# Optimization experiments

Measured on AMD Instinct MI355X. Metric: run time of the kernel, lower is better.

Reference implementation:

```python
import jax, jax.numpy as jnp
import numpy as np

K, D = 8, 32          # num_heads, node_out_dim
KD = K * D            # 256
NEG = 0.2             # LeakyReLU negative slope
N, E = 100000, 300000
DIN, DREL = 128, 64


def setup_inputs() -> dict:
    key = jax.random.key(0)
    ks = iter(jax.random.split(key, 64))
    def nrm(shape, scale):
        return jax.random.normal(next(ks), shape, jnp.float32) * scale
    inp = {}
    # per-relation target-node features feats[(s,e,d)] : (N_d, d_in)
    for nm in ["feat_ui", "feat_iu", "feat_ii", "feat_ii_rev"]:
        inp[nm] = nrm((N, DIN), 1.0)
    # relation input features (d_rel,)
    for nm in ["r_ui", "r_iu", "r_ii", "r_ii_rev"]:
        inp[nm] = nrm((DREL,), 1.0)
    # fc_node per ntype (no bias), shared for src/dst roles
    inp["W_user"] = nrm((DIN, KD), 0.05)
    inp["W_item"] = nrm((DIN, KD), 0.05)
    # fc_rel per etype (no bias): d_rel -> 2*K*d
    for nm in ["Wrel_ui", "Wrel_iu", "Wrel_ii", "Wrel_ii_rev"]:
        inp[nm] = nrm((DREL, 2 * KD), 0.05)
    # cross-relation attention vectors (K, d)
    for nm in ["attn_ui", "attn_iu", "attn_ii", "attn_ii_rev"]:
        inp[nm] = nrm((K, D), 0.1)
    # residual fc per ntype (with bias) and residual gate scalar
    inp["Wres_user"] = nrm((DIN, KD), 0.05); inp["bres_user"] = nrm((KD,), 0.02)
    inp["Wres_item"] = nrm((DIN, KD), 0.05); inp["bres_item"] = nrm((KD,), 0.02)
    inp["a_user"] = jax.random.uniform(next(ks), (1,), jnp.float32)
    inp["a_item"] = jax.random.uniform(next(ks), (1,), jnp.float32)
    # fc_upd per etype (with bias): d_rel -> K*rel_out
    for nm in ["ui", "iu", "ii", "ii_rev"]:
        inp["Wupd_" + nm] = nrm((DREL, KD), 0.05)
        inp["bupd_" + nm] = nrm((KD,), 0.02)
    # edge lists per relation
    for nm in ["ui", "iu", "ii", "ii_rev"]:
        inp["src_" + nm] = jax.random.randint(next(ks), (E,), 0, N, jnp.int32)
        inp["dst_" + nm] = jax.random.randint(next(ks), (E,), 0, N, jnp.int32)
    return inp


def _conv(fsrc_in, fdst_in, Ws, Wd, Wrel, rfeat, src, dst):
    """RelationGraphConv: GAT-style attention over one bipartite relation."""
    n_dst = fdst_in.shape[0]
    fs = (fsrc_in @ Ws).reshape(-1, K, D)          # (Ns, K, D)
    fd = (fdst_in @ Wd).reshape(-1, K, D)          # (Nd, K, D)
    attn = (rfeat @ Wrel).reshape(K, 2 * D)        # (K, 2D)
    el = (fs * attn[:, :D]).sum(-1)                # (Ns, K)
    er = (fd * attn[:, D:]).sum(-1)                # (Nd, K)
    e = jax.nn.leaky_relu(el[src] + er[dst], NEG)  # (E, K)
    # edge softmax per destination node
    m = jax.ops.segment_max(e, dst, num_segments=n_dst)
    ex = jnp.exp(e - m[dst])
    s = jax.ops.segment_sum(ex, dst, num_segments=n_dst)
    a = ex / s[dst]                                # (E, K)
    msg = fs[src] * a[:, :, None]                  # (E, K, D)
    out = jax.ops.segment_sum(msg, dst, num_segments=n_dst)
    return jax.nn.relu(out.reshape(n_dst, KD))     # activation = relu


def _crossing(stacked, rel_attn):
    """RelationCrossing over stacked per-relation dst reps (R, N, K*D)."""
    R, Nn = stacked.shape[0], stacked.shape[1]
    f = stacked.reshape(R, Nn, K, D)
    sc = (rel_attn * f).sum(-1, keepdims=True)             # (R, N, K, 1)
    sc = jax.nn.softmax(jax.nn.leaky_relu(sc, NEG), axis=0)
    return (sc * f).sum(0).reshape(Nn, KD)


def reference(feat_ui, feat_iu, feat_ii, feat_ii_rev,
              r_ui, r_iu, r_ii, r_ii_rev,
              W_user, W_item,
              Wrel_ui, Wrel_iu, Wrel_ii, Wrel_ii_rev,
              attn_ui, attn_iu, attn_ii, attn_ii_rev,
              Wres_user, bres_user, Wres_item, bres_item,
              a_user, a_item,
              Wupd_ui, bupd_ui, Wupd_iu, bupd_iu,
              Wupd_ii, bupd_ii, Wupd_ii_rev, bupd_ii_rev,
              src_ui, dst_ui, src_iu, dst_iu,
              src_ii, dst_ii, src_ii_rev, dst_ii_rev):
    # relation convs; src feats come from the reverse relation's dict entry
    h_ui = _conv(feat_iu, feat_ui, W_user, W_item, Wrel_ui, r_ui, src_ui, dst_ui)
    h_iu = _conv(feat_ui, feat_iu, W_item, W_user, Wrel_iu, r_iu, src_iu, dst_iu)
    h_ii = _conv(feat_ii_rev, feat_ii, W_item, W_item, Wrel_ii, r_ii, src_ii, dst_ii)
    h_iir = _conv(feat_ii, feat_ii_rev, W_item, W_item, Wrel_ii_rev, r_ii_rev, src_ii_rev, dst_ii_rev)

    # gated residual per dtype
    def resid(h, fdst, Wres, bres, a):
        al = jax.nn.sigmoid(a)
        return al * h + (1.0 - al) * (fdst @ Wres + bres)

    h_ui = resid(h_ui, feat_ui, Wres_item, bres_item, a_item)
    h_iu = resid(h_iu, feat_iu, Wres_user, bres_user, a_user)
    h_ii = resid(h_ii, feat_ii, Wres_item, bres_item, a_item)
    h_iir = resid(h_iir, feat_ii_rev, Wres_item, bres_item, a_item)

    # cross-relation fusion: dtype item has relations [ui, ii, ii_rev]; user has [iu]
    item_stack = jnp.stack([h_ui, h_ii, h_iir], axis=0)
    out_ui = _crossing(item_stack, attn_ui)
    out_iu = h_iu  # num_rel == 1 -> identity
    out_ii = _crossing(item_stack, attn_ii)
    out_iir = _crossing(item_stack, attn_ii_rev)

    # relation feature update
    ro_ui = r_ui @ Wupd_ui + bupd_ui
    ro_iu = r_iu @ Wupd_iu + bupd_iu
    ro_ii = r_ii @ Wupd_ii + bupd_ii
    ro_iir = r_ii_rev @ Wupd_ii_rev + bupd_ii_rev
    return (out_ui, out_iu, out_ii, out_iir, ro_ui, ro_iu, ro_ii, ro_iir)
```

## Files before the change

kernel.cpp:

```cpp
#include <hip/hip_runtime.h>
#include <hip/hip_bf16.h>
#include <math.h>

#define NEG_SLOPE 0.2f
#define LOG2E 1.4426950408889634f

using bf16x8 = __attribute__((ext_vector_type(8))) short;
using f32x4  = __attribute__((ext_vector_type(4))) float;
using u16x8  = __attribute__((ext_vector_type(8))) unsigned short;
using u16x4  = __attribute__((ext_vector_type(4))) unsigned short;

__device__ __forceinline__ float lrelu(float x) { return x > 0.f ? x : NEG_SLOPE * x; }
__device__ __forceinline__ float dot4(float4 a, float4 b) {
    return a.x * b.x + a.y * b.y + a.z * b.z + a.w * b.w;
}
__device__ __forceinline__ unsigned short f2b(float x) {
    union { float f; unsigned u; } v; v.f = x;
    unsigned r = v.u + 0x7fff + ((v.u >> 16) & 1);
    return (unsigned short)(r >> 16);
}
__device__ __forceinline__ float b2f(unsigned short b) {
    union { unsigned u; float f; } v; v.u = ((unsigned)b) << 16;
    return v.f;
}
__device__ __forceinline__ float4 load4b(const unsigned short* p) {
    u16x4 u = *reinterpret_cast<const u16x4*>(p);
    return make_float4(b2f(u[0]), b2f(u[1]), b2f(u[2]), b2f(u[3]));
}
__device__ __forceinline__ bf16x8 cvt8(float4 a0, float4 a1) {
    union { u16x8 u; bf16x8 b; } c;
    c.u[0] = f2b(a0.x); c.u[1] = f2b(a0.y); c.u[2] = f2b(a0.z); c.u[3] = f2b(a0.w);
    c.u[4] = f2b(a1.x); c.u[5] = f2b(a1.y); c.u[6] = f2b(a1.z); c.u[7] = f2b(a1.w);
    return c.b;
}

struct PackArgs {
    const float* W1[4];
    const float* W2[4];
    const float* wvA[4];
    const float* wvB[4];
    unsigned short* Bp[4];
};

__global__ __launch_bounds__(256)
void pack_b_k(PackArgs pa)
{
    const int r = blockIdx.y;
    const int nb = blockIdx.x;
    const int ks = threadIdx.x >> 6;
    const int lane = threadIdx.x & 63;
    const int n = nb * 16 + (lane & 15);
    const int k0 = ks * 32 + (lane >> 4) * 8;
    u16x8 u;
    if (n < 512) {
        const float* Wsrc = (n < 256) ? (pa.W1[r] + n) : (pa.W2[r] + (n - 256));
        #pragma unroll
        for (int e = 0; e < 8; ++e) u[e] = f2b(Wsrc[(size_t)(k0 + e) * 256]);
    } else {
        const int h = (n - 512) & 7;
        const bool isEr = (n >= 520);
        const float* wv = isEr ? (pa.wvB[r] + h * 64 + 32) : (pa.wvA[r] + h * 64);
        const float* Wc = pa.W1[r] + h * 32;
        #pragma unroll
        for (int e = 0; e < 8; ++e) {
            const size_t k = (size_t)(k0 + e);
            float s = 0.f;
            #pragma unroll 8
            for (int d = 0; d < 32; ++d) s = fmaf(Wc[k * 256 + d], wv[d], s);
            u[e] = f2b(s);
        }
    }
    const size_t gid = (size_t)((nb * 4 + ks) * 64 + lane);
    *reinterpret_cast<u16x8*>(pa.Bp[r] + gid * 8) = u;
}

struct GemmArgs {
    const float* A[4];
    const unsigned short* Bp[4];
    const float* bres[4];
    unsigned short* pool[4];
    unsigned short* resid[4];
    float* elOut[4];
    float* erOut[4];
};

__global__ __launch_bounds__(256)
void mfma_gemm_k(GemmArgs ga, int Nrows)
{
    __shared__ __align__(16) char smem[49152];
    unsigned short* slab = (unsigned short*)smem;
    char* bounce = smem + 32768;
    const int rsel = blockIdx.y;
    const int t = threadIdx.x;
    const int wv = t >> 6, lane = t & 63;
    const int l15 = lane & 15, lg = lane >> 4;
    const int nloc = wv * 16 + l15;
    const int m0 = blockIdx.x * 64;
    const int node = m0 + nloc;
    const bool valid = node < Nrows;
    const int nc = valid ? node : (Nrows - 1);

    const float* __restrict__ A = ga.A[rsel];
    const unsigned short* __restrict__ Bp = ga.Bp[rsel];
    const float* __restrict__ bres = ga.bres[rsel];

    bf16x8 bfr[4];
    #pragma unroll
    for (int ks = 0; ks < 4; ++ks) {
        const float* p = A + (size_t)nc * 128 + ks * 32 + lg * 8;
        float4 a0 = *reinterpret_cast<const float4*>(p);
        float4 a1 = *reinterpret_cast<const float4*>(p + 4);
        bfr[ks] = cvt8(a0, a1);
    }

    const int swz = (nloc & 7) << 4;

    u16x8 sreg[8];
    #pragma unroll
    for (int j = 0; j < 8; ++j)
        sreg[j] = *reinterpret_cast<const u16x8*>(Bp + (size_t)(j * 256 + t) * 8);

    u16x8 snext;

    #pragma unroll
    for (int p = 0; p < 4; ++p) {
        #pragma unroll
        for (int j = 0; j < 8; ++j)
            *reinterpret_cast<u16x8*>(slab + (size_t)(j * 256 + t) * 8) = sreg[j];
        __syncthreads();
        if (p < 3) {
            const unsigned short* src = Bp + (size_t)(p + 1) * 16384;
            #pragma unroll
            for (int j = 0; j < 8; ++j)
                sreg[j] = *reinterpret_cast<const u16x8*>(src + (size_t)(j * 256 + t) * 8);
        } else {
            snext = *reinterpret_cast<const u16x8*>(Bp + (size_t)65536 + (size_t)t * 8);
        }
        const bool isPool = (p < 2);
        #pragma unroll
        for (int i = 0; i < 8; ++i) {
            f32x4 acc = (f32x4){0.f, 0.f, 0.f, 0.f};
            #pragma unroll
            for (int ks = 0; ks < 4; ++ks) {
                bf16x8 wf = *reinterpret_cast<const bf16x8*>(
                    slab + (size_t)((i * 4 + ks) * 64 + lane) * 8);
                acc = __builtin_amdgcn_mfma_f32_16x16x32_bf16(wf, bfr[ks], acc, 0, 0, 0);
            }
            u16x4 o;
            if (isPool) {
                o[0] = f2b(acc[0]); o[1] = f2b(acc[1]);
                o[2] = f2b(acc[2]); o[3] = f2b(acc[3]);
            } else {
                const int cb = (p - 2) * 128 + i * 16 + lg * 4;
                float4 bv = *reinterpret_cast<const float4*>(bres + cb);
                o[0] = f2b(acc[0] + bv.x); o[1] = f2b(acc[1] + bv.y);
                o[2] = f2b(acc[2] + bv.z); o[3] = f2b(acc[3] + bv.w);
            }
            *reinterpret_cast<u16x4*>(bounce + nloc * 256 + ((i * 32 + lg * 8) ^ swz)) = o;
        }
        __syncthreads();
        {
            unsigned short* __restrict__ dst = isPool ? ga.pool[rsel] : ga.resid[rsel];
            const int colbase = (p & 1) * 128;
            #pragma unroll
            for (int it = 0; it < 4; ++it) {
                const int chunk = it * 256 + t;
                const int row = chunk >> 4;
                const int c16 = chunk & 15;
                const int byte = row * 256 + ((c16 * 16) ^ ((row & 7) << 4));
                u16x8 v = *reinterpret_cast<const u16x8*>(bounce + byte);
                if (m0 + row < Nrows)
                    *reinterpret_cast<u16x8*>(dst + (size_t)(m0 + row) * 256
                                              + colbase + c16 * 8) = v;
            }
        }
    }
    *reinterpret_cast<u16x8*>(slab + (size_t)t * 8) = snext;
    __syncthreads();
    {
        f32x4 acc = (f32x4){0.f, 0.f, 0.f, 0.f};
        #pragma unroll
        for (int ks = 0; ks < 4; ++ks) {
            bf16x8 wf = *reinterpret_cast<const bf16x8*>(
                slab + (size_t)(ks * 64 + lane) * 8);
            acc = __builtin_amdgcn_mfma_f32_16x16x32_bf16(wf, bfr[ks], acc, 0, 0, 0);
        }
        if (valid) {
            float4 v = make_float4(acc[0], acc[1], acc[2], acc[3]);
            if (lg < 2)
                *reinterpret_cast<float4*>(ga.elOut[rsel] + (size_t)node * 8 + lg * 4) = v;
            else
                *reinterpret_cast<float4*>(ga.erOut[rsel] + (size_t)node * 8 + (lg - 2) * 4) = v;
        }
    }
}

struct EdgePtrs {
    const int* src[4];
    const int* dst[4];
    int E[4];
    int csrOff[4];
};

__global__ __launch_bounds__(256)
void hist_k(EdgePtrs ep, int* __restrict__ counts4, int N)
{
    const int r = blockIdx.y;
    const int e = blockIdx.x * 256 + threadIdx.x;
    if (e < ep.E[r]) atomicAdd(counts4 + (size_t)r * N + ep.dst[r][e], 1);
}

__global__ __launch_bounds__(256)
void blksum_k(const int* __restrict__ counts4, int* __restrict__ blksum4, int N)
{
    const int r = blockIdx.y;
    const int* c = counts4 + (size_t)r * N;
    const int base = blockIdx.x * 1024 + threadIdx.x;
    int s = 0;
    #pragma unroll
    for (int i = 0; i < 4; ++i) { int idx = base + i * 256; if (idx < N) s += c[idx]; }
    __shared__ int sd[256];
    sd[threadIdx.x] = s; __syncthreads();
    for (int off = 128; off > 0; off >>= 1) {
        if (threadIdx.x < off) sd[threadIdx.x] += sd[threadIdx.x + off];
        __syncthreads();
    }
    if (threadIdx.x == 0) blksum4[r * 1024 + blockIdx.x] = sd[0];
}

__global__ __launch_bounds__(1024)
void scanblk_k(int* __restrict__ blksum4, int nbx)
{
    const int r = blockIdx.x;
    const int t = threadIdx.x;
    __shared__ int sd[1024];
    int v = (t < nbx) ? blksum4[r * 1024 + t] : 0;
    sd[t] = v; __syncthreads();
    for (int off = 1; off < 1024; off <<= 1) {
        int u = (t >= off) ? sd[t - off] : 0;
        __syncthreads();
        sd[t] += u;
        __syncthreads();
    }
    if (t < nbx) blksum4[r * 1024 + t] = sd[t] - v;
}

__global__ __launch_bounds__(256)
void cursor_k(const int* __restrict__ counts4, const int* __restrict__ blkoff4,
              int* __restrict__ cursor4, int N)
{
    const int r = blockIdx.y;
    const int* c = counts4 + (size_t)r * N;
    int* cur = cursor4 + (size_t)r * N;
    const int t = threadIdx.x;
    const int base = blockIdx.x * 1024 + t * 4;
    const int c0 = (base + 0 < N) ? c[base + 0] : 0;
    const int c1 = (base + 1 < N) ? c[base + 1] : 0;
    const int c2 = (base + 2 < N) ? c[base + 2] : 0;
    const int c3 = (base + 3 < N) ? c[base + 3] : 0;
    const int tsum = c0 + c1 + c2 + c3;
    __shared__ int sd[256];
    sd[t] = tsum; __syncthreads();
    for (int off = 1; off < 256; off <<= 1) {
        int u = (t >= off) ? sd[t - off] : 0;
        __syncthreads();
        sd[t] += u;
        __syncthreads();
    }
    int excl = sd[t] - tsum + blkoff4[r * 1024 + blockIdx.x];
    if (base + 0 < N) cur[base + 0] = excl;
    if (base + 1 < N) cur[base + 1] = excl + c0;
    if (base + 2 < N) cur[base + 2] = excl + c0 + c1;
    if (base + 3 < N) cur[base + 3] = excl + c0 + c1 + c2;
}

__global__ __launch_bounds__(256)
void scatter_k(EdgePtrs ep, int* __restrict__ cursor4, int* __restrict__ csr_src, int N)
{
    const int r = blockIdx.y;
    const int e = blockIdx.x * 256 + threadIdx.x;
    if (e < ep.E[r]) {
        const int d = ep.dst[r][e];
        const int pos = atomicAdd(cursor4 + (size_t)r * N + d, 1);
        csr_src[ep.csrOff[r] + pos] = ep.src[r][e];
    }
}

struct NodeArgs {
    const int* csr[4];
    const int* cursor[4];
    const int* counts[4];
    const float* el[4];
    const float* er[4];
    const unsigned short* pool[4];
    const unsigned short* resid[4];
};

__global__ __launch_bounds__(256)
void node_k(NodeArgs na,
            const float* __restrict__ attn_ui, const float* __restrict__ attn_ii,
            const float* __restrict__ attn_iir,
            const float* __restrict__ a_user, const float* __restrict__ a_item,
            float* __restrict__ out, int Nrows)
{
    const int lane = threadIdx.x & 63;
    const int n = blockIdx.x * 4 + (threadIdx.x >> 6);
    if (n >= Nrows) return;
    const unsigned k = (unsigned)(lane >> 3);
    const unsigned c4 = (unsigned)(lane * 4);

    int deg[4], start[4];
    float erk[4];
    #pragma unroll
    for (int r = 0; r < 4; ++r) {
        deg[r]  = na.counts[r][n];
        const int endv = na.cursor[r][n];
        start[r] = endv - deg[r];
        erk[r]  = na.er[r][(size_t)n * 8 + k];
    }

    const float si = 1.f / (1.f + __expf(-a_item[0])), osi = 1.f - si;
    const float su = 1.f / (1.f + __expf(-a_user[0])), osu = 1.f - su;

    float4 fr[4];
    #pragma unroll
    for (int r = 0; r < 4; ++r) {
        const int d = deg[r];
        const int st = start[r];
        const int* __restrict__ csr = na.csr[r];
        const float* __restrict__ elr = na.el[r];
        const unsigned short* __restrict__ fs = na.pool[r];
        const float er_k = erk[r];
        float s = 0.f;
        float4 acc = make_float4(0.f, 0.f, 0.f, 0.f);
        for (int base = 0; base < d; base += 4) {
            const int m = d - base;
            int sidx[4];
            #pragma unroll
            for (int u = 0; u < 4; ++u)
                sidx[u] = csr[st + base + ((u < m) ? u : 0)];
            float ex[4];
            #pragma unroll
            for (int u = 0; u < 4; ++u) {
                const float x = elr[(unsigned)sidx[u] * 8u + k] + er_k;
                const float e = __builtin_amdgcn_exp2f(fmaxf(x, NEG_SLOPE * x));
                ex[u] = (u < m) ? e : 0.f;
            }
            float4 pv[4];
            #pragma unroll
            for (int u = 0; u < 4; ++u)
                pv[u] = load4b(fs + (unsigned)sidx[u] * 256u + c4);
            #pragma unroll
            for (int u = 0; u < 4; ++u) {
                s += ex[u];
                acc.x = fmaf(pv[u].x, ex[u], acc.x);
                acc.y = fmaf(pv[u].y, ex[u], acc.y);
                acc.z = fmaf(pv[u].z, ex[u], acc.z);
                acc.w = fmaf(pv[u].w, ex[u], acc.w);
            }
        }
        const float inv = (d > 0) ? 1.f / s : 0.f;
        float4 R = load4b(na.resid[r] + (unsigned)n * 256u + c4);
        const float sg = (r == 1) ? su : si;
        const float og = (r == 1) ? osu : osi;
        fr[r].x = sg * fmaxf(acc.x * inv, 0.f) + og * R.x;
        fr[r].y = sg * fmaxf(acc.y * inv, 0.f) + og * R.y;
        fr[r].z = sg * fmaxf(acc.z * inv, 0.f) + og * R.z;
        fr[r].w = sg * fmaxf(acc.w * inv, 0.f) + og * R.w;
    }

    const float4 f0 = fr[0], f1 = fr[2], f2 = fr[3], fiu = fr[1];
    float4 w0 = *reinterpret_cast<const float4*>(attn_ui  + lane * 4);
    float4 w1 = *reinterpret_cast<const float4*>(attn_ii  + lane * 4);
    float4 w2 = *reinterpret_cast<const float4*>(attn_iir + lane * 4);

    float p[3][3];
    p[0][0] = dot4(w0, f0); p[0][1] = dot4(w0, f1); p[0][2] = dot4(w0, f2);
    p[1][0] = dot4(w1, f0); p[1][1] = dot4(w1, f1); p[1][2] = dot4(w1, f2);
    p[2][0] = dot4(w2, f0); p[2][1] = dot4(w2, f1); p[2][2] = dot4(w2, f2);
    #pragma unroll
    for (int x = 0; x < 3; ++x)
        #pragma unroll
        for (int r = 0; r < 3; ++r)
            #pragma unroll
            for (int m = 1; m < 8; m <<= 1)
                p[x][r] += __shfl_xor(p[x][r], m, 64);

    const size_t NK = (size_t)Nrows * 256;
    const size_t o = (size_t)n * 256 + lane * 4;
    const size_t xoff[3] = {0, 2 * NK, 3 * NK};
    #pragma unroll
    for (int x = 0; x < 3; ++x) {
        float a0 = lrelu(p[x][0]), a1 = lrelu(p[x][1]), a2 = lrelu(p[x][2]);
        float mx = fmaxf(a0, fmaxf(a1, a2));
        float e0 = __expf(a0 - mx), e1 = __expf(a1 - mx), e2 = __expf(a2 - mx);
        float inv = 1.f / (e0 + e1 + e2);
        e0 *= inv; e1 *= inv; e2 *= inv;
        float4 rr;
        rr.x = e0 * f0.x + e1 * f1.x + e2 * f2.x;
        rr.y = e0 * f0.y + e1 * f1.y + e2 * f2.y;
        rr.z = e0 * f0.z + e1 * f1.z + e2 * f2.z;
        rr.w = e0 * f0.w + e1 * f1.w + e2 * f2.w;
        *reinterpret_cast<float4*>(out + xoff[x] + o) = rr;
    }
    *reinterpret_cast<float4*>(out + NK + o) = fiu;
}

struct RelPtrs {
    const float* rf[4];
    const float* Wrel[4];
    const float* Wupd[4];
    const float* bupd[4];
};

__global__ __launch_bounds__(512)
void rel_k(RelPtrs P, float* __restrict__ wvec, float* __restrict__ ro)
{
    const int r = blockIdx.x;
    const int t = threadIdx.x;
    __shared__ float rfs[64];
    if (t < 64) rfs[t] = P.rf[r][t];
    __syncthreads();
    {
        const float* Wc = P.Wrel[r];
        float acc = 0.f;
        #pragma unroll 8
        for (int i = 0; i < 64; ++i) acc = fmaf(rfs[i], Wc[(size_t)i * 512 + t], acc);
        wvec[(size_t)r * 512 + t] = acc * LOG2E;
    }
    if (t < 256) {
        const float* Wc = P.Wupd[r];
        float acc = P.bupd[r][t];
        #pragma unroll 8
        for (int i = 0; i < 64; ++i) acc = fmaf(rfs[i], Wc[(size_t)i * 256 + t], acc);
        ro[(size_t)r * 256 + t] = acc;
    }
}

extern "C" void kernel_launch(void* const* d_in, const int* in_sizes, int n_in,
                              void* d_out, int out_size, void* d_ws, size_t ws_size,
                              hipStream_t stream)
{
    (void)n_in; (void)out_size; (void)ws_size;
    const float* feat_ui  = (const float*)d_in[0];
    const float* feat_iu  = (const float*)d_in[1];
    const float* feat_ii  = (const float*)d_in[2];
    const float* feat_iir = (const float*)d_in[3];
    const float* W_user   = (const float*)d_in[8];
    const float* W_item   = (const float*)d_in[9];
    const float* Wres_user = (const float*)d_in[18];
    const float* bres_user = (const float*)d_in[19];
    const float* Wres_item = (const float*)d_in[20];
    const float* bres_item = (const float*)d_in[21];
    const float* a_user = (const float*)d_in[22];
    const float* a_item = (const float*)d_in[23];
    const int N = in_sizes[0] / 128;
    const int Es[4] = {in_sizes[32], in_sizes[34], in_sizes[36], in_sizes[38]};
    int maxE = 0;
    for (int r = 0; r < 4; ++r) maxE = Es[r] > maxE ? Es[r] : maxE;

    const size_t NP = (size_t)N * 256;
    const size_t N8 = (size_t)N * 8;
    const size_t BPSZ = 33 * 4 * 64 * 8;

    unsigned short* us = (unsigned short*)d_ws;
    unsigned short* pool[4];
    unsigned short* resid[4];
    for (int r = 0; r < 4; ++r) pool[r]  = us + (size_t)r * NP;
    for (int r = 0; r < 4; ++r) resid[r] = us + (size_t)(4 + r) * NP;
    unsigned short* BpArr[4];
    for (int r = 0; r < 4; ++r) BpArr[r] = us + 8 * NP + (size_t)r * BPSZ;
    float* fl = (float*)(us + 8 * NP + 4 * BPSZ);
    float *el[4], *er[4];
    for (int r = 0; r < 4; ++r) { el[r] = fl + (size_t)(2 * r) * N8; er[r] = fl + (size_t)(2 * r + 1) * N8; }
    float* wvec = fl + 8 * N8;
    int* counts4 = (int*)(wvec + 4 * 512);
    int* cursor4 = counts4 + 4 * (size_t)N;
    int* blksum4 = cursor4 + 4 * (size_t)N;
    int* csr_src = blksum4 + 4 * 1024;
    float* out = (float*)d_out;

    EdgePtrs ep;
    {
        int off = 0;
        const int si[4] = {32, 34, 36, 38};
        for (int r = 0; r < 4; ++r) {
            ep.src[r] = (const int*)d_in[si[r]];
            ep.dst[r] = (const int*)d_in[si[r] + 1];
            ep.E[r] = Es[r];
            ep.csrOff[r] = off;
            off += Es[r];
        }
    }

    (void)hipMemsetAsync(counts4, 0, 4 * (size_t)N * sizeof(int), stream);

    RelPtrs rp;
    rp.rf[0]   = (const float*)d_in[4];  rp.rf[1]   = (const float*)d_in[5];
    rp.rf[2]   = (const float*)d_in[6];  rp.rf[3]   = (const float*)d_in[7];
    rp.Wrel[0] = (const float*)d_in[10]; rp.Wrel[1] = (const float*)d_in[11];
    rp.Wrel[2] = (const float*)d_in[12]; rp.Wrel[3] = (const float*)d_in[13];
    rp.Wupd[0] = (const float*)d_in[24]; rp.Wupd[1] = (const float*)d_in[26];
    rp.Wupd[2] = (const float*)d_in[28]; rp.Wupd[3] = (const float*)d_in[30];
    rp.bupd[0] = (const float*)d_in[25]; rp.bupd[1] = (const float*)d_in[27];
    rp.bupd[2] = (const float*)d_in[29]; rp.bupd[3] = (const float*)d_in[31];
    rel_k<<<dim3(4), dim3(512), 0, stream>>>(rp, wvec, out + 4 * NP);

    const int pair[4] = {1, 0, 3, 2};
    PackArgs pa;
    pa.W1[0] = W_user; pa.W2[0] = Wres_user;
    pa.W1[1] = W_item; pa.W2[1] = Wres_item;
    pa.W1[2] = W_item; pa.W2[2] = Wres_item;
    pa.W1[3] = W_item; pa.W2[3] = Wres_item;
    for (int r = 0; r < 4; ++r) {
        pa.wvA[r] = wvec + (size_t)r * 512;
        pa.wvB[r] = wvec + (size_t)pair[r] * 512;
        pa.Bp[r]  = BpArr[r];
    }
    pack_b_k<<<dim3(33, 4), 256, 0, stream>>>(pa);

    const int geb = (maxE + 255) / 256;
    const int nbx = (N + 1023) / 1024;
    hist_k<<<dim3(geb, 4), 256, 0, stream>>>(ep, counts4, N);
    blksum_k<<<dim3(nbx, 4), 256, 0, stream>>>(counts4, blksum4, N);
    scanblk_k<<<dim3(4), 1024, 0, stream>>>(blksum4, nbx);
    cursor_k<<<dim3(nbx, 4), 256, 0, stream>>>(counts4, blksum4, cursor4, N);
    scatter_k<<<dim3(geb, 4), 256, 0, stream>>>(ep, cursor4, csr_src, N);

    GemmArgs ga;
    ga.A[0] = feat_iu;  ga.bres[0] = bres_user;
    ga.A[1] = feat_ui;  ga.bres[1] = bres_item;
    ga.A[2] = feat_iir; ga.bres[2] = bres_item;
    ga.A[3] = feat_ii;  ga.bres[3] = bres_item;
    for (int r = 0; r < 4; ++r) {
        ga.Bp[r]    = BpArr[r];
        ga.pool[r]  = pool[r];
        ga.resid[r] = resid[pair[r]];
        ga.elOut[r] = el[r];
        ga.erOut[r] = er[pair[r]];
    }
    const int gb = (N + 63) / 64;
    mfma_gemm_k<<<dim3(gb, 4), 256, 0, stream>>>(ga, N);

    NodeArgs na;
    for (int r = 0; r < 4; ++r) {
        na.csr[r]    = csr_src + ep.csrOff[r];
        na.cursor[r] = cursor4 + (size_t)r * N;
        na.counts[r] = counts4 + (size_t)r * N;
        na.el[r]     = el[r];
        na.er[r]     = er[r];
        na.pool[r]   = pool[r];
        na.resid[r]  = resid[r];
    }
    const int nb4 = (N + 3) / 4;
    node_k<<<nb4, 256, 0, stream>>>(na,
                                    (const float*)d_in[14], (const float*)d_in[16],
                                    (const float*)d_in[17],
                                    a_user, a_item, out, N);
}
```

Measured before the change: 557.8 us.

## Split node aggregation across two wavefronts per node, combine via shared memory

The node kernel now assigns two wavefronts to each destination node, each aggregating two of the four relations, instead of one wavefront walking all four relations serially. The per-relation results are exchanged through shared memory after a block barrier, and one wavefront per node then does the cross-relation attention and output. This exposes more parallelism and memory-level concurrency for the gather-heavy aggregation. In exchange it adds LDS traffic and a __syncthreads, doubles the grid size, and leaves half the wavefronts idle during the epilogue.

```diff
diff --git a/kernel.cpp b/kernel.cpp
--- a/kernel.cpp
+++ b/kernel.cpp
@@ -303,73 +303,86 @@
             const float* __restrict__ a_user, const float* __restrict__ a_item,
             float* __restrict__ out, int Nrows)
 {
-    const int lane = threadIdx.x & 63;
-    const int n = blockIdx.x * 4 + (threadIdx.x >> 6);
-    if (n >= Nrows) return;
+    __shared__ float frs[2][4][256];
+    const int t = threadIdx.x;
+    const int w = t >> 6;
+    const int lane = t & 63;
+    const int nslot = w >> 1;
+    const int rbase = (w & 1) * 2;
+    const int n = blockIdx.x * 2 + nslot;
+    const bool nvalid = n < Nrows;
     const unsigned k = (unsigned)(lane >> 3);
     const unsigned c4 = (unsigned)(lane * 4);
 
-    int deg[4], start[4];
-    float erk[4];
-    #pragma unroll
-    for (int r = 0; r < 4; ++r) {
-        deg[r]  = na.counts[r][n];
-        const int endv = na.cursor[r][n];
-        start[r] = endv - deg[r];
-        erk[r]  = na.er[r][(size_t)n * 8 + k];
-    }
-
     const float si = 1.f / (1.f + __expf(-a_item[0])), osi = 1.f - si;
     const float su = 1.f / (1.f + __expf(-a_user[0])), osu = 1.f - su;
 
-    float4 fr[4];
-    #pragma unroll
-    for (int r = 0; r < 4; ++r) {
-        const int d = deg[r];
-        const int st = start[r];
-        const int* __restrict__ csr = na.csr[r];
-        const float* __restrict__ elr = na.el[r];
-        const unsigned short* __restrict__ fs = na.pool[r];
-        const float er_k = erk[r];
-        float s = 0.f;
-        float4 acc = make_float4(0.f, 0.f, 0.f, 0.f);
-        for (int base = 0; base < d; base += 4) {
-            const int m = d - base;
-            int sidx[4];
-            #pragma unroll
-            for (int u = 0; u < 4; ++u)
-                sidx[u] = csr[st + base + ((u < m) ? u : 0)];
-            float ex[4];
-            #pragma unroll
-            for (int u = 0; u < 4; ++u) {
-                const float x = elr[(unsigned)sidx[u] * 8u + k] + er_k;
-                const float e = __builtin_amdgcn_exp2f(fmaxf(x, NEG_SLOPE * x));
-                ex[u] = (u < m) ? e : 0.f;
+    if (nvalid) {
+        int deg[2], start[2];
+        float erk[2];
+        #pragma unroll
+        for (int rr = 0; rr < 2; ++rr) {
+            const int r = rbase + rr;
+            deg[rr]  = na.counts[r][n];
+            start[rr] = na.cursor[r][n] - deg[rr];
+            erk[rr]  = na.er[r][(size_t)n * 8 + k];
+        }
+        #pragma unroll
+        for (int rr = 0; rr < 2; ++rr) {
+            const int r = rbase + rr;
+            const int d = deg[rr];
+            const int st = start[rr];
+            const int* __restrict__ csr = na.csr[r];
+            const float* __restrict__ elr = na.el[r];
+            const unsigned short* __restrict__ fs = na.pool[r];
+            const float er_k = erk[rr];
+            float s = 0.f;
+            float4 acc = make_float4(0.f, 0.f, 0.f, 0.f);
+            for (int base = 0; base < d; base += 4) {
+                const int m = d - base;
+                int sidx[4];
+                #pragma unroll
+                for (int u = 0; u < 4; ++u)
+                    sidx[u] = csr[st + base + ((u < m) ? u : 0)];
+                float ex[4];
+                #pragma unroll
+                for (int u = 0; u < 4; ++u) {
+                    const float x = elr[(unsigned)sidx[u] * 8u + k] + er_k;
+                    const float e = __builtin_amdgcn_exp2f(fmaxf(x, NEG_SLOPE * x));
+                    ex[u] = (u < m) ? e : 0.f;
+                }
+                float4 pv[4];
+                #pragma unroll
+                for (int u = 0; u < 4; ++u)
+                    pv[u] = load4b(fs + (unsigned)sidx[u] * 256u + c4);
+                #pragma unroll
+                for (int u = 0; u < 4; ++u) {
+                    s += ex[u];
+                    acc.x = fmaf(pv[u].x, ex[u], acc.x);
+                    acc.y = fmaf(pv[u].y, ex[u], acc.y);
+                    acc.z = fmaf(pv[u].z, ex[u], acc.z);
+                    acc.w = fmaf(pv[u].w, ex[u], acc.w);
+                }
             }
-            float4 pv[4];
-            #pragma unroll
-            for (int u = 0; u < 4; ++u)
-                pv[u] = load4b(fs + (unsigned)sidx[u] * 256u + c4);
-            #pragma unroll
-            for (int u = 0; u < 4; ++u) {
-                s += ex[u];
-                acc.x = fmaf(pv[u].x, ex[u], acc.x);
-                acc.y = fmaf(pv[u].y, ex[u], acc.y);
-                acc.z = fmaf(pv[u].z, ex[u], acc.z);
-                acc.w = fmaf(pv[u].w, ex[u], acc.w);
-            }
-        }
-        const float inv = (d > 0) ? 1.f / s : 0.f;
-        float4 R = load4b(na.resid[r] + (unsigned)n * 256u + c4);
-        const float sg = (r == 1) ? su : si;
-        const float og = (r == 1) ? osu : osi;
-        fr[r].x = sg * fmaxf(acc.x * inv, 0.f) + og * R.x;
-        fr[r].y = sg * fmaxf(acc.y * inv, 0.f) + og * R.y;
-        fr[r].z = sg * fmaxf(acc.z * inv, 0.f) + og * R.z;
-        fr[r].w = sg * fmaxf(acc.w * inv, 0.f) + og * R.w;
-    }
-
-    const float4 f0 = fr[0], f1 = fr[2], f2 = fr[3], fiu = fr[1];
+            const float inv = (d > 0) ? 1.f / s : 0.f;
+            float4 R = load4b(na.resid[r] + (unsigned)n * 256u + c4);
+            const float sg = (r == 1) ? su : si;
+            const float og = (r == 1) ? osu : osi;
+            float4 frv;
+            frv.x = sg * fmaxf(acc.x * inv, 0.f) + og * R.x;
+            frv.y = sg * fmaxf(acc.y * inv, 0.f) + og * R.y;
+            frv.z = sg * fmaxf(acc.z * inv, 0.f) + og * R.z;
+            frv.w = sg * fmaxf(acc.w * inv, 0.f) + og * R.w;
+            *reinterpret_cast<float4*>(&frs[nslot][r][c4]) = frv;
+        }
+    }
+    __syncthreads();
+    if ((w & 1) != 0 || !nvalid) return;
+
+    const float4 f0  = *reinterpret_cast<const float4*>(&frs[nslot][0][c4]);
+    const float4 fiu = *reinterpret_cast<const float4*>(&frs[nslot][1][c4]);
+    const float4 f1  = *reinterpret_cast<const float4*>(&frs[nslot][2][c4]);
+    const float4 f2  = *reinterpret_cast<const float4*>(&frs[nslot][3][c4]);
     float4 w0 = *reinterpret_cast<const float4*>(attn_ui  + lane * 4);
     float4 w1 = *reinterpret_cast<const float4*>(attn_ii  + lane * 4);
     float4 w2 = *reinterpret_cast<const float4*>(attn_iir + lane * 4);
@@ -552,8 +565,8 @@
         na.pool[r]   = pool[r];
         na.resid[r]  = resid[r];
     }
-    const int nb4 = (N + 3) / 4;
-    node_k<<<nb4, 256, 0, stream>>>(na,
+    const int nb2 = (N + 1) / 2;
+    node_k<<<nb2, 256, 0, stream>>>(na,
                                     (const float*)d_in[14], (const float*)d_in[16],
                                     (const float*)d_in[17],
                                     a_user, a_item, out, N);
```

Result: slower. 682.8 us (+22.4%).
